# Performance work log

Measured on AMD Instinct MI355X. Metric: run time of the kernel, lower is better.

Reference implementation:

```python
import jax, jax.numpy as jnp
import numpy as np

BN_EPS = 1e-5

def _conv1d(x, w, b, pad):
    # x: [B, C_in, L], w: [C_out, C_in, K]
    y = jax.lax.conv_general_dilated(x, w, (1,), [(pad, pad)],
                                     dimension_numbers=('NCH', 'OIH', 'NCH'))
    return y + b[None, :, None]

def _gru_dir(x, wih, whh, bih, bhh, reverse):
    # x: [B, L, I]; wih: [3H, I]; whh: [3H, H] (PyTorch GRU gate order r,z,n)
    H = whh.shape[1]
    gx = jnp.einsum('bli,gi->blg', x, wih) + bih  # [B, L, 3H]
    gx = jnp.swapaxes(gx, 0, 1)                    # [L, B, 3H]
    if reverse:
        gx = gx[::-1]
    def step(h, xt):
        gh = h @ whh.T + bhh
        xr, xz, xn = jnp.split(xt, 3, axis=-1)
        hr, hz, hn = jnp.split(gh, 3, axis=-1)
        r = jax.nn.sigmoid(xr + hr)
        z = jax.nn.sigmoid(xz + hz)
        n = jnp.tanh(xn + r * hn)
        h = (1 - z) * n + z * h
        return h, h
    h0 = jnp.zeros((x.shape[0], H), x.dtype)
    _, hs = jax.lax.scan(step, h0, gx)
    if reverse:
        hs = hs[::-1]
    return jnp.swapaxes(hs, 0, 1)  # [B, L, H]

def _bigru(x, wih, whh, bih, bhh):
    f = _gru_dir(x, wih[0], whh[0], bih[0], bhh[0], False)
    b = _gru_dir(x, wih[1], whh[1], bih[1], bhh[1], True)
    return jnp.concatenate([f, b], axis=-1)

def _bn_eval(x, gamma, beta):
    # eval-mode BatchNorm1d with running_mean=0, running_var=1
    return x / jnp.sqrt(1.0 + BN_EPS) * gamma + beta

def _forward(wd_emb, pos_emb, conv_w2, conv_b2, conv_w3, conv_b3, conv_w4, conv_b4,
             wd_wih0, wd_whh0, wd_bih0, wd_bhh0, wd_wih1, wd_whh1, wd_bih1, wd_bhh1,
             pos_wih0, pos_whh0, pos_bih0, pos_bhh0, pos_wih1, pos_whh1, pos_bih1, pos_bhh1,
             squish_w, atten_proj, posfc_gamma, posfc_beta, posfc_w, posfc_b,
             fc1_w, fc1_b, fc_gamma, fc_beta, fc2_w, fc2_b, wd, pos):
    we = wd_emb[wd]    # [B, L, D]
    pe = pos_emb[pos]  # [B, L, D]
    x = jnp.swapaxes(we, 1, 2)  # [B, D, L]
    L = x.shape[-1]
    # parallel conv branches, truncated to min length L, concat -> 144 channels
    c2 = _conv1d(x, conv_w2, conv_b2, 1)[:, :, :L]
    c3 = _conv1d(x, conv_w3, conv_b3, 1)[:, :, :L]
    c4 = _conv1d(x, conv_w4, conv_b4, 2)[:, :, :L]
    feat = jnp.swapaxes(jnp.concatenate([c2, c3, c4], axis=1), 1, 2)  # [B, L, 144]
    # 2-layer bidirectional GRUs (hidden=3; dropout disabled at eval)
    wd_out = _bigru(_bigru(feat, wd_wih0, wd_whh0, wd_bih0, wd_bhh0),
                    wd_wih1, wd_whh1, wd_bih1, wd_bhh1)   # [B, L, 6]
    pos_out = _bigru(_bigru(pe, pos_wih0, pos_whh0, pos_bih0, pos_bhh0),
                     pos_wih1, pos_whh1, pos_bih1, pos_bhh1)  # [B, L, 6]
    # word attention (vectorized version of batch_matmul/attention_matmul loops)
    squish = jnp.tanh(wd_out @ squish_w)        # [B, L, 6]
    att = squish @ atten_proj                    # [B, L, 1]
    attn = jax.nn.softmax(att, axis=1)           # softmax over seq dim
    wd_atten = jnp.sum(wd_out * attn, axis=1)    # [B, 6]
    # auxiliary pos head
    ph = jax.nn.relu(_bn_eval(pos_out[:, -1, :], posfc_gamma, posfc_beta))
    auxi = jax.nn.softmax(ph @ posfc_w.T + posfc_b, axis=-1)  # [B, 3]
    # main head
    comb = jnp.concatenate([wd_atten, auxi], axis=1)  # [B, 9]
    h = jax.nn.relu(_bn_eval(comb @ fc1_w.T + fc1_b, fc_gamma, fc_beta))
    logits = jax.nn.softmax(h @ fc2_w.T + fc2_b, axis=-1)     # [B, 6]
    return logits, auxi

def setup_inputs() -> dict:
    key = jax.random.key(0)
    B, L, D, H, V, P = 512, 512, 100, 3, 23757, 57
    G = 3 * H  # 9
    keys = iter(jax.random.split(key, 48))
    def nrm(shape, s=0.1):
        return jax.random.normal(next(keys), shape, jnp.float32) * s
    inp = {}
    inp['wd'] = jax.random.randint(next(keys), (B, L), 0, V)
    inp['pos'] = jax.random.randint(next(keys), (B, L), 0, P)
    inp['wd_emb'] = nrm((V, D), 1.0)
    inp['pos_emb'] = nrm((P, D), 1.0)
    inp['conv_w2'] = nrm((48, D, 2)); inp['conv_b2'] = nrm((48,))
    inp['conv_w3'] = nrm((48, D, 3)); inp['conv_b3'] = nrm((48,))
    inp['conv_w4'] = nrm((48, D, 4)); inp['conv_b4'] = nrm((48,))
    inp['wd_wih0'] = nrm((2, G, 144)); inp['wd_whh0'] = nrm((2, G, H))
    inp['wd_bih0'] = nrm((2, G));      inp['wd_bhh0'] = nrm((2, G))
    inp['wd_wih1'] = nrm((2, G, 2 * H)); inp['wd_whh1'] = nrm((2, G, H))
    inp['wd_bih1'] = nrm((2, G));        inp['wd_bhh1'] = nrm((2, G))
    inp['pos_wih0'] = nrm((2, G, D));    inp['pos_whh0'] = nrm((2, G, H))
    inp['pos_bih0'] = nrm((2, G));       inp['pos_bhh0'] = nrm((2, G))
    inp['pos_wih1'] = nrm((2, G, 2 * H)); inp['pos_whh1'] = nrm((2, G, H))
    inp['pos_bih1'] = nrm((2, G));        inp['pos_bhh1'] = nrm((2, G))
    inp['squish_w'] = nrm((2 * H, 2 * H), 1.0)
    inp['atten_proj'] = nrm((2 * H, 1), 1.0)
    inp['posfc_gamma'] = jnp.ones((2 * H,), jnp.float32)
    inp['posfc_beta'] = jnp.zeros((2 * H,), jnp.float32)
    inp['posfc_w'] = nrm((3, 2 * H)); inp['posfc_b'] = nrm((3,))
    inp['fc1_w'] = nrm((128, 9)); inp['fc1_b'] = nrm((128,))
    inp['fc_gamma'] = jnp.ones((128,), jnp.float32)
    inp['fc_beta'] = jnp.zeros((128,), jnp.float32)
    inp['fc2_w'] = nrm((6, 128)); inp['fc2_b'] = nrm((6,))
    return inp

def reference(wd, pos, wd_emb, pos_emb, conv_w2, conv_b2, conv_w3, conv_b3, conv_w4, conv_b4,
              wd_wih0, wd_whh0, wd_bih0, wd_bhh0, wd_wih1, wd_whh1, wd_bih1, wd_bhh1,
              pos_wih0, pos_whh0, pos_bih0, pos_bhh0, pos_wih1, pos_whh1, pos_bih1, pos_bhh1,
              squish_w, atten_proj, posfc_gamma, posfc_beta, posfc_w, posfc_b,
              fc1_w, fc1_b, fc_gamma, fc_beta, fc2_w, fc2_b):
    return _forward(wd_emb, pos_emb, conv_w2, conv_b2, conv_w3, conv_b3, conv_w4, conv_b4,
                    wd_wih0, wd_whh0, wd_bih0, wd_bhh0, wd_wih1, wd_whh1, wd_bih1, wd_bhh1,
                    pos_wih0, pos_whh0, pos_bih0, pos_bhh0, pos_wih1, pos_whh1, pos_bih1, pos_bhh1,
                    squish_w, atten_proj, posfc_gamma, posfc_beta, posfc_w, posfc_b,
                    fc1_w, fc1_b, fc_gamma, fc_beta, fc2_w, fc2_b, wd, pos)
```

## Files before the change

kernel.cpp:

```cpp
#include <hip/hip_runtime.h>
#include <hip/hip_fp16.h>
#include <math.h>

#define BB 512
#define LL 512
#define VV 23757
#define PP 57

#define L2E  1.4426950408889634f
#define NL2E (-1.4426950408889634f)
#define TL2E 2.8853900817779268f

__device__ __forceinline__ float rcp_(float x) { return __builtin_amdgcn_rcpf(x); }
__device__ __forceinline__ float exp2_(float x) { return __builtin_amdgcn_exp2f(x); }
__device__ __forceinline__ float tanh_(float x) { return 1.f - 2.f * rcp_(exp2_(TL2E * x) + 1.f); }

__device__ __forceinline__ float gscale(int dg) {
    int g = (dg % 9) / 3;
    return g == 2 ? TL2E : NL2E;
}
__device__ __forceinline__ int is_rz(int dg) { return ((dg % 9) / 3) < 2; }

template <int K>
__device__ __forceinline__ float qb(float x) {
    constexpr int ctrl = K * 0x55;
    return __int_as_float(__builtin_amdgcn_update_dpp(0, __float_as_int(x), ctrl, 0xF, 0xF, true));
}

struct F3 { float r, z, n; };
struct H4 { __half2 a, b; };

__global__ void k_build_tables(const float* __restrict__ wd_wih0, const float* __restrict__ wd_bih0,
                               const float* __restrict__ wd_bhh0,
                               const float* __restrict__ cw2, const float* __restrict__ cb2,
                               const float* __restrict__ cw3, const float* __restrict__ cb3,
                               const float* __restrict__ cw4, const float* __restrict__ cb4,
                               const float* __restrict__ pos_emb,
                               const float* __restrict__ pos_wih0, const float* __restrict__ pos_bih0,
                               const float* __restrict__ pos_bhh0,
                               const float* __restrict__ wd_wih1, const float* __restrict__ wd_bih1,
                               const float* __restrict__ wd_bhh1,
                               const float* __restrict__ pos_wih1, const float* __restrict__ pos_bih1,
                               const float* __restrict__ pos_bhh1,
                               float* __restrict__ E, float* __restrict__ beff, float* __restrict__ Gp,
                               float* __restrict__ wih1t, float* __restrict__ bih1t)
{
    int idx = blockIdx.x * blockDim.x + threadIdx.x;
    if (idx < 7200) {
        int d  = idx % 100;
        int tt = (idx / 100) % 4;
        int dg = idx / 400;
        const float* wih = wd_wih0 + dg * 144;
        float acc = 0.f;
        if (tt == 0) {
            for (int o = 0; o < 48; ++o) acc += wih[96 + o] * cw4[o * 400 + d * 4 + 0];
        } else if (tt == 1) {
            for (int o = 0; o < 48; ++o) acc += wih[o]      * cw2[o * 200 + d * 2 + 0];
            for (int o = 0; o < 48; ++o) acc += wih[48 + o] * cw3[o * 300 + d * 3 + 0];
            for (int o = 0; o < 48; ++o) acc += wih[96 + o] * cw4[o * 400 + d * 4 + 1];
        } else if (tt == 2) {
            for (int o = 0; o < 48; ++o) acc += wih[o]      * cw2[o * 200 + d * 2 + 1];
            for (int o = 0; o < 48; ++o) acc += wih[48 + o] * cw3[o * 300 + d * 3 + 1];
            for (int o = 0; o < 48; ++o) acc += wih[96 + o] * cw4[o * 400 + d * 4 + 2];
        } else {
            for (int o = 0; o < 48; ++o) acc += wih[48 + o] * cw3[o * 300 + d * 3 + 2];
            for (int o = 0; o < 48; ++o) acc += wih[96 + o] * cw4[o * 400 + d * 4 + 3];
        }
        E[idx] = acc;
    } else if (idx < 7218) {
        int dg = idx - 7200;
        float acc = wd_bih0[dg];
        for (int o = 0; o < 48; ++o) acc += wd_wih0[dg * 144 + o]      * cb2[o];
        for (int o = 0; o < 48; ++o) acc += wd_wih0[dg * 144 + 48 + o] * cb3[o];
        for (int o = 0; o < 48; ++o) acc += wd_wih0[dg * 144 + 96 + o] * cb4[o];
        if (is_rz(dg)) acc += wd_bhh0[dg];
        beff[dg] = gscale(dg) * acc;
    } else if (idx < 8244) {
        int k = idx - 7218;
        int dg = k % 18;
        int p  = k / 18;
        float acc = pos_bih0[dg];
        for (int d = 0; d < 100; ++d) acc += pos_emb[p * 100 + d] * pos_wih0[dg * 100 + d];
        if (is_rz(dg)) acc += pos_bhh0[dg];
        Gp[p * 18 + dg] = gscale(dg) * acc;
    } else if (idx < 8352) {
        int i = idx - 8244; int dg = i / 6;
        wih1t[i] = gscale(dg) * wd_wih1[i];
    } else if (idx < 8370) {
        int dg = idx - 8352;
        float a = wd_bih1[dg] + (is_rz(dg) ? wd_bhh1[dg] : 0.f);
        bih1t[dg] = gscale(dg) * a;
    } else if (idx < 8478) {
        int i = idx - 8370; int dg = i / 6;
        wih1t[108 + i] = gscale(dg) * pos_wih1[i];
    } else if (idx < 8496) {
        int dg = idx - 8478;
        float a = pos_bih1[dg] + (is_rz(dg) ? pos_bhh1[dg] : 0.f);
        bih1t[18 + dg] = gscale(dg) * a;
    }
}

__global__ void __launch_bounds__(256) k_build_P(const float* __restrict__ wd_emb,
                                                 const float* __restrict__ E,
                                                 __half* __restrict__ P16)
{
    __shared__ float sEt[7200];
    for (int i = threadIdx.x; i < 7200; i += 256) {
        int d = i % 100, r = i / 100;
        int tt = r / 18, dg = r % 18;
        sEt[d * 72 + r] = E[dg * 400 + tt * 100 + d];
    }
    __syncthreads();
    int T = blockIdx.x * 256 + threadIdx.x;
    int og = T & 7;
    int vb = T >> 3;
    int v0 = vb * 4;
    if (v0 >= VV) return;
    int vlim = VV - 1 - v0;
    float gs[9];
#pragma unroll
    for (int k = 0; k < 9; ++k) {
        int dg = (og * 9 + k) % 18;
        gs[k] = ((dg % 9) / 3 == 2) ? TL2E : NL2E;
    }
    float acc[4][9];
#pragma unroll
    for (int vi = 0; vi < 4; ++vi)
#pragma unroll
        for (int k = 0; k < 9; ++k) acc[vi][k] = 0.f;

    const float* e0 = wd_emb + (size_t)v0 * 100;
#pragma unroll 1
    for (int d4 = 0; d4 < 25; ++d4) {
        float4 ev[4];
#pragma unroll
        for (int vi = 0; vi < 4; ++vi) {
            int vv = vi <= vlim ? vi : vlim;
            ev[vi] = *(const float4*)(e0 + vv * 100 + d4 * 4);
        }
#pragma unroll
        for (int dd = 0; dd < 4; ++dd) {
            int d = d4 * 4 + dd;
            const float* et = sEt + d * 72 + og * 9;
            float em0 = ((const float*)&ev[0])[dd];
            float em1 = ((const float*)&ev[1])[dd];
            float em2 = ((const float*)&ev[2])[dd];
            float em3 = ((const float*)&ev[3])[dd];
#pragma unroll
            for (int k = 0; k < 9; ++k) {
                float e = et[k];
                acc[0][k] = fmaf(em0, e, acc[0][k]);
                acc[1][k] = fmaf(em1, e, acc[1][k]);
                acc[2][k] = fmaf(em2, e, acc[2][k]);
                acc[3][k] = fmaf(em3, e, acc[3][k]);
            }
        }
    }
#pragma unroll
    for (int vi = 0; vi < 4; ++vi) {
        if (vi <= vlim) {
            __half* p = P16 + (size_t)(v0 + vi) * 72 + og * 9;
#pragma unroll
            for (int k = 0; k < 9; ++k) p[k] = __float2half_rn(gs[k] * acc[vi][k]);
        }
    }
}

__global__ void k_gather(const int* __restrict__ wd, const int* __restrict__ pos,
                         const __half* __restrict__ P16, const float* __restrict__ beff,
                         const float* __restrict__ Gp, char* __restrict__ gxh)
{
    int idx = blockIdx.x * blockDim.x + threadIdx.x;
    if (idx >= 2 * BB * LL) return;
    int branch = idx >= BB * LL;
    int k = idx - branch * BB * LL;
    int l = k % LL, b = k / LL;

    float v[18];
    if (!branch) {
#pragma unroll
        for (int i = 0; i < 18; ++i) v[i] = beff[i];
        const int* row = wd + b * LL;
#pragma unroll
        for (int t = 0; t < 4; ++t) {
            int ll = l - 2 + t;
            if (ll >= 0 && ll < LL) {
                const __half2* p = (const __half2*)(P16 + (size_t)row[ll] * 72 + t * 18);
#pragma unroll
                for (int i = 0; i < 9; ++i) {
                    float2 f = __half22float2(p[i]);
                    v[2 * i] += f.x;
                    v[2 * i + 1] += f.y;
                }
            }
        }
    } else {
        const float* p = Gp + pos[k] * 18;
#pragma unroll
        for (int i = 0; i < 18; ++i) v[i] = p[i];
    }
    char* g0 = gxh + ((size_t)((branch * 2 + 0) * BB + b) * LL + l) * 24;
    char* g1 = gxh + ((size_t)((branch * 2 + 1) * BB + b) * LL + l) * 24;
#pragma unroll
    for (int j = 0; j < 3; ++j) {
        H4 w0, w1;
        w0.a = __floats2half2_rn(v[j], v[3 + j]);
        w0.b = __floats2half2_rn(v[6 + j], 0.f);
        w1.a = __floats2half2_rn(v[9 + j], v[12 + j]);
        w1.b = __floats2half2_rn(v[15 + j], 0.f);
        *(H4*)(g0 + j * 8) = w0;
        *(H4*)(g1 + j * 8) = w1;
    }
}

#define GRU_CORE(GR, GZ, GN)                                                  \
    {                                                                         \
        float h0_ = qb<0>(h), h1_ = qb<1>(h), h2_ = qb<2>(h);                 \
        float sr_ = fmaf(wr0, h0_, fmaf(wr1, h1_, fmaf(wr2, h2_, (GR))));     \
        float sz_ = fmaf(wz0, h0_, fmaf(wz1, h1_, fmaf(wz2, h2_, (GZ))));     \
        float g3_ = fmaf(wn0, h0_, fmaf(wn1, h1_, fmaf(wn2, h2_, bnx)));      \
        float r_ = rcp_(1.f + exp2_(sr_));                                    \
        float z_ = rcp_(1.f + exp2_(sz_));                                    \
        float u_ = rcp_(1.f + exp2_(fmaf(r_, g3_, (GN))));                    \
        float n_ = fmaf(-2.f, u_, 1.f);                                       \
        h = fmaf(z_, h - n_, n_);                                             \
    }

__global__ void __launch_bounds__(64) k_scan0(
        const char* __restrict__ gxh, char* __restrict__ out0h,
        const float* __restrict__ whhA, const float* __restrict__ bhhA,
        const float* __restrict__ whhB, const float* __restrict__ bhhB)
{
    __shared__ float lbuf[8 * 81];
    int lane = threadIdx.x;
    int c = lane >> 2, sub = lane & 3;
    int jj = sub < 3 ? sub : 2;
    int chain = blockIdx.x;
    int branch = chain >> 10;
    int rem = chain & 1023;
    int dir = rem >> 9;

    const float* whh = (branch ? whhB : whhA) + dir * 27;
    const float* bhh = (branch ? bhhB : bhhA) + dir * 9;

    float wr0 = NL2E * whh[jj * 3 + 0], wr1 = NL2E * whh[jj * 3 + 1], wr2 = NL2E * whh[jj * 3 + 2];
    float wz0 = NL2E * whh[(3 + jj) * 3 + 0], wz1 = NL2E * whh[(3 + jj) * 3 + 1], wz2 = NL2E * whh[(3 + jj) * 3 + 2];
    float wn0 = TL2E * whh[(6 + jj) * 3 + 0], wn1 = TL2E * whh[(6 + jj) * 3 + 1], wn2 = TL2E * whh[(6 + jj) * 3 + 2];
    float bnx = TL2E * bhh[6 + jj];

    const int OMAX = 511 * 24;
    int t0 = c * 32 - 24;
    int sstp = dir ? -24 : 24;
    int off = dir ? (OMAX - t0 * 24) : t0 * 24;
    const char* gxc = gxh + (size_t)chain * (LL * 24) + jj * 8;

#define LDP(P) { int a_ = min(max(off, 0), OMAX); P = *(const H4*)(gxc + a_); off += sstp; }
    H4 p0, p1, p2, p3, p4, p5, p6, p7;
    LDP(p0) LDP(p1) LDP(p2) LDP(p3) LDP(p4) LDP(p5) LDP(p6) LDP(p7)

    char* ob = out0h + (size_t)chain * (LL * 8) + sub * 16;
    int wa = c * 5 + sub;

    float h = 0.f;
#define WSTEP(P) { H4 hv_ = P; LDP(P); float2 fa_ = __half22float2(hv_.a); \
                   float fn_ = __half22float2(hv_.b).x; GRU_CORE(fa_.x, fa_.y, fn_) }
#define RSTEP(P, S) { WSTEP(P) lbuf[(S) * 81 + wa] = h; }
#define FLUSH0(TB)                                                            \
    {                                                                         \
        int tbase = (TB);                                                     \
        int l0 = dir ? (LL - 1 - tbase - 7) : tbase;                          \
        _Pragma("unroll")                                                     \
        for (int i = 0; i < 2; ++i) {                                         \
            int lofs = sub * 2 + i;                                           \
            int s = dir ? (7 - lofs) : lofs;                                  \
            H4 hv;                                                            \
            hv.a = __floats2half2_rn(lbuf[s * 81 + c * 5 + 0],                \
                                     lbuf[s * 81 + c * 5 + 1]);               \
            hv.b = __floats2half2_rn(lbuf[s * 81 + c * 5 + 2],                \
                                     lbuf[s * 81 + c * 5 + 3]);               \
            *(H4*)(ob + (size_t)l0 * 8 + i * 8) = hv;                         \
        }                                                                     \
    }

    for (int g = 0; g < 3; ++g) {
        WSTEP(p0) WSTEP(p1) WSTEP(p2) WSTEP(p3) WSTEP(p4) WSTEP(p5) WSTEP(p6) WSTEP(p7)
    }
    h = c ? h : 0.f;

    for (int g = 0; g < 4; ++g) {
        RSTEP(p0, 0) RSTEP(p1, 1) RSTEP(p2, 2) RSTEP(p3, 3)
        RSTEP(p4, 4) RSTEP(p5, 5) RSTEP(p6, 6) RSTEP(p7, 7)
        FLUSH0(t0 + 24 + g * 8)
    }
#undef LDP
#undef WSTEP
#undef RSTEP
#undef FLUSH0
}

__global__ void __launch_bounds__(64) k_scan1(
        const char* __restrict__ out0h, char* __restrict__ out1h,
        const float* __restrict__ whhA, const float* __restrict__ bhhA,
        const float* __restrict__ whhB, const float* __restrict__ bhhB,
        const float* __restrict__ wih1t, const float* __restrict__ bih1t)
{
    __shared__ float lbuf[8 * 81];
    int lane = threadIdx.x;
    int c = lane >> 2, sub = lane & 3;
    int jj = sub < 3 ? sub : 2;
    int chain = blockIdx.x;
    int branch = chain >> 10;
    int rem = chain & 1023;
    int dir = rem >> 9;
    int b = rem & 511;

    const float* whh = (branch ? whhB : whhA) + dir * 27;
    const float* bhh = (branch ? bhhB : bhhA) + dir * 9;

    float wr0 = NL2E * whh[jj * 3 + 0], wr1 = NL2E * whh[jj * 3 + 1], wr2 = NL2E * whh[jj * 3 + 2];
    float wz0 = NL2E * whh[(3 + jj) * 3 + 0], wz1 = NL2E * whh[(3 + jj) * 3 + 1], wz2 = NL2E * whh[(3 + jj) * 3 + 2];
    float wn0 = TL2E * whh[(6 + jj) * 3 + 0], wn1 = TL2E * whh[(6 + jj) * 3 + 1], wn2 = TL2E * whh[(6 + jj) * 3 + 2];
    float bnx = TL2E * bhh[6 + jj];

    const float* Wb = wih1t + branch * 108;
    const float* Bv = bih1t + branch * 18;
    int dgr = dir * 9 + jj, dgz = dgr + 3, dgn = dgr + 6;
    float Wr0 = Wb[dgr * 6 + 0], Wr1 = Wb[dgr * 6 + 1], Wr2 = Wb[dgr * 6 + 2];
    float Wr3 = Wb[dgr * 6 + 3], Wr4 = Wb[dgr * 6 + 4], Wr5 = Wb[dgr * 6 + 5];
    float Wz0 = Wb[dgz * 6 + 0], Wz1 = Wb[dgz * 6 + 1], Wz2 = Wb[dgz * 6 + 2];
    float Wz3 = Wb[dgz * 6 + 3], Wz4 = Wb[dgz * 6 + 4], Wz5 = Wb[dgz * 6 + 5];
    float Wn0 = Wb[dgn * 6 + 0], Wn1 = Wb[dgn * 6 + 1], Wn2 = Wb[dgn * 6 + 2];
    float Wn3 = Wb[dgn * 6 + 3], Wn4 = Wb[dgn * 6 + 4], Wn5 = Wb[dgn * 6 + 5];
    float Br = Bv[dgr], Bz = Bv[dgz], Bn = Bv[dgn];

    const char* o0c = out0h + (size_t)((branch * 2 + 0) * BB + b) * (LL * 8);
    const char* o1c = out0h + (size_t)((branch * 2 + 1) * BB + b) * (LL * 8);

    const int OMAX = 511 * 8;
    int t0 = c * 32 - 24;
    int sstp = dir ? -8 : 8;
    int off = dir ? (OMAX - t0 * 8) : t0 * 8;

#define LDF(F, Q) { int a_ = min(max(off, 0), OMAX); F = *(const H4*)(o0c + a_); \
                    Q = *(const H4*)(o1c + a_); off += sstp; }
    H4 f0, f1, f2, f3, f4, f5, f6, f7;
    H4 q0, q1, q2, q3, q4, q5, q6, q7;
    LDF(f0, q0) LDF(f1, q1) LDF(f2, q2) LDF(f3, q3)
    LDF(f4, q4) LDF(f5, q5) LDF(f6, q6) LDF(f7, q7)

    char* ob = out1h + (size_t)chain * (LL * 8) + sub * 16;
    int wa = c * 5 + sub;

    float h = 0.f;
#define PRJ_STEP(FV, QV)                                                      \
    {                                                                         \
        float2 fa_ = __half22float2((FV).a);                                  \
        float fn_ = __half22float2((FV).b).x;                                 \
        float2 qa_ = __half22float2((QV).a);                                  \
        float qn_ = __half22float2((QV).b).x;                                 \
        float gr_ = fmaf(fa_.x, Wr0, fmaf(fa_.y, Wr1, fmaf(fn_, Wr2, Br)));   \
        gr_ = fmaf(qa_.x, Wr3, fmaf(qa_.y, Wr4, fmaf(qn_, Wr5, gr_)));        \
        float gz_ = fmaf(fa_.x, Wz0, fmaf(fa_.y, Wz1, fmaf(fn_, Wz2, Bz)));   \
        gz_ = fmaf(qa_.x, Wz3, fmaf(qa_.y, Wz4, fmaf(qn_, Wz5, gz_)));        \
        float gn_ = fmaf(fa_.x, Wn0, fmaf(fa_.y, Wn1, fmaf(fn_, Wn2, Bn)));   \
        gn_ = fmaf(qa_.x, Wn3, fmaf(qa_.y, Wn4, fmaf(qn_, Wn5, gn_)));        \
        GRU_CORE(gr_, gz_, gn_)                                               \
    }
#define WSTEP(F, Q) { H4 fv_ = F, qv_ = Q; LDF(F, Q); PRJ_STEP(fv_, qv_) }
#define RSTEP(F, Q, S) { WSTEP(F, Q) lbuf[(S) * 81 + wa] = h; }
#define FLUSH1(TB)                                                            \
    {                                                                         \
        int tbase = (TB);                                                     \
        int l0 = dir ? (LL - 1 - tbase - 7) : tbase;                          \
        _Pragma("unroll")                                                     \
        for (int i = 0; i < 2; ++i) {                                         \
            int lofs = sub * 2 + i;                                           \
            int s = dir ? (7 - lofs) : lofs;                                  \
            H4 hv;                                                            \
            hv.a = __floats2half2_rn(lbuf[s * 81 + c * 5 + 0],                \
                                     lbuf[s * 81 + c * 5 + 1]);               \
            hv.b = __floats2half2_rn(lbuf[s * 81 + c * 5 + 2],                \
                                     lbuf[s * 81 + c * 5 + 3]);               \
            *(H4*)(ob + (size_t)l0 * 8 + i * 8) = hv;                         \
        }                                                                     \
    }

    for (int g = 0; g < 3; ++g) {
        WSTEP(f0, q0) WSTEP(f1, q1) WSTEP(f2, q2) WSTEP(f3, q3)
        WSTEP(f4, q4) WSTEP(f5, q5) WSTEP(f6, q6) WSTEP(f7, q7)
    }
    h = c ? h : 0.f;

    for (int g = 0; g < 4; ++g) {
        RSTEP(f0, q0, 0) RSTEP(f1, q1, 1) RSTEP(f2, q2, 2) RSTEP(f3, q3, 3)
        RSTEP(f4, q4, 4) RSTEP(f5, q5, 5) RSTEP(f6, q6, 6) RSTEP(f7, q7, 7)
        FLUSH1(t0 + 24 + g * 8)
    }
#undef LDF
#undef PRJ_STEP
#undef WSTEP
#undef RSTEP
#undef FLUSH1
}

__global__ void k_head(const char* __restrict__ out1h,
                       const float* __restrict__ sw, const float* __restrict__ ap,
                       const float* __restrict__ pg, const float* __restrict__ pb,
                       const float* __restrict__ pw, const float* __restrict__ pbias,
                       const float* __restrict__ f1w, const float* __restrict__ f1b,
                       const float* __restrict__ fg, const float* __restrict__ fb,
                       const float* __restrict__ f2w, const float* __restrict__ f2b,
                       float* __restrict__ out)
{
    int b = blockIdx.x;
    int lane = threadIdx.x;
    __shared__ float ssw[36], sap[6], sph[6], scomb[9], sh[128], sl[6], se[6];
    const float BN = 0.9999950000374997f;

    if (lane < 36) ssw[lane] = sw[lane];
    if (lane < 6) {
        sap[lane] = ap[lane];
        H4 pf = *(const H4*)(out1h + ((size_t)((2 * BB) + b) * LL + 511) * 8);
        H4 pq = *(const H4*)(out1h + ((size_t)((3 * BB) + b) * LL + 511) * 8);
        float2 fa = __half22float2(pf.a); float fn = __half22float2(pf.b).x;
        float2 ba = __half22float2(pq.a); float bn = __half22float2(pq.b).x;
        float v = lane == 0 ? fa.x : lane == 1 ? fa.y : lane == 2 ? fn
                : lane == 3 ? ba.x : lane == 4 ? ba.y : bn;
        float x = v * BN * pg[lane] + pb[lane];
        sph[lane] = fmaxf(x, 0.f);
    }
    __syncthreads();

    const char* F = out1h + (size_t)b * (LL * 8);
    const char* Bw = out1h + (size_t)(BB + b) * (LL * 8);

    float att[8];
    float mx = -1e30f;
#pragma unroll
    for (int k = 0; k < 8; ++k) {
        int l = lane + 64 * k;
        H4 f4 = *(const H4*)(F + l * 8);
        H4 b4 = *(const H4*)(Bw + l * 8);
        float2 fa = __half22float2(f4.a); float fn = __half22float2(f4.b).x;
        float2 ba = __half22float2(b4.a); float bn = __half22float2(b4.b).x;
        float r0 = fa.x, r1 = fa.y, r2 = fn, r3 = ba.x, r4 = ba.y, r5 = bn;
        float a = 0.f;
#pragma unroll
        for (int j = 0; j < 6; ++j) {
            float s = r0 * ssw[0 * 6 + j] + r1 * ssw[1 * 6 + j] + r2 * ssw[2 * 6 + j] +
                      r3 * ssw[3 * 6 + j] + r4 * ssw[4 * 6 + j] + r5 * ssw[5 * 6 + j];
            a += sap[j] * tanh_(s);
        }
        att[k] = a;
        mx = fmaxf(mx, a);
    }
#pragma unroll
    for (int off = 32; off; off >>= 1) mx = fmaxf(mx, __shfl_xor(mx, off));
    float e[8];
    float sum = 0.f;
#pragma unroll
    for (int k = 0; k < 8; ++k) { e[k] = exp2_(L2E * (att[k] - mx)); sum += e[k]; }
#pragma unroll
    for (int off = 32; off; off >>= 1) sum += __shfl_xor(sum, off);

    float acc[6] = {0.f, 0.f, 0.f, 0.f, 0.f, 0.f};
#pragma unroll
    for (int k = 0; k < 8; ++k) {
        int l = lane + 64 * k;
        H4 f4 = *(const H4*)(F + l * 8);
        H4 b4 = *(const H4*)(Bw + l * 8);
        float2 fa = __half22float2(f4.a); float fn = __half22float2(f4.b).x;
        float2 ba = __half22float2(b4.a); float bn = __half22float2(b4.b).x;
        acc[0] += e[k] * fa.x; acc[1] += e[k] * fa.y; acc[2] += e[k] * fn;
        acc[3] += e[k] * ba.x; acc[4] += e[k] * ba.y; acc[5] += e[k] * bn;
    }
#pragma unroll
    for (int j = 0; j < 6; ++j) {
#pragma unroll
        for (int off = 32; off; off >>= 1) acc[j] += __shfl_xor(acc[j], off);
    }
    if (lane < 6) scomb[lane] = acc[lane] / sum;
    __syncthreads();

    if (lane == 0) {
        float a[3];
#pragma unroll
        for (int j = 0; j < 3; ++j) {
            float t = pbias[j];
#pragma unroll
            for (int i = 0; i < 6; ++i) t += sph[i] * pw[j * 6 + i];
            a[j] = t;
        }
        float m = fmaxf(a[0], fmaxf(a[1], a[2]));
        float e0 = exp2_(L2E * (a[0] - m)), e1 = exp2_(L2E * (a[1] - m)), e2 = exp2_(L2E * (a[2] - m));
        float s = e0 + e1 + e2;
        float x0 = e0 / s, x1 = e1 / s, x2 = e2 / s;
        scomb[6] = x0; scomb[7] = x1; scomb[8] = x2;
        out[BB * 6 + b * 3 + 0] = x0;
        out[BB * 6 + b * 3 + 1] = x1;
        out[BB * 6 + b * 3 + 2] = x2;
    }
    __syncthreads();
    for (int o = lane; o < 128; o += 64) {
        float t = f1b[o];
#pragma unroll
        for (int k = 0; k < 9; ++k) t += scomb[k] * f1w[o * 9 + k];
        float x = t * BN * fg[o] + fb[o];
        sh[o] = fmaxf(x, 0.f);
    }
    __syncthreads();
    if (lane < 6) {
        float t = f2b[lane];
        for (int k = 0; k < 128; ++k) t += sh[k] * f2w[lane * 128 + k];
        sl[lane] = t;
    }
    __syncthreads();
    if (lane < 6) {
        float m = sl[0];
#pragma unroll
        for (int j = 1; j < 6; ++j) m = fmaxf(m, sl[j]);
        se[lane] = exp2_(L2E * (sl[lane] - m));
    }
    __syncthreads();
    if (lane < 6) {
        float s = se[0] + se[1] + se[2] + se[3] + se[4] + se[5];
        out[b * 6 + lane] = se[lane] / s;
    }
}

extern "C" void kernel_launch(void* const* d_in, const int* in_sizes, int n_in,
                              void* d_out, int out_size, void* d_ws, size_t ws_size,
                              hipStream_t stream)
{
    const int* wd  = (const int*)d_in[0];
    const int* pos = (const int*)d_in[1];
    const float* wd_emb  = (const float*)d_in[2];
    const float* pos_emb = (const float*)d_in[3];
    const float* cw2 = (const float*)d_in[4];  const float* cb2 = (const float*)d_in[5];
    const float* cw3 = (const float*)d_in[6];  const float* cb3 = (const float*)d_in[7];
    const float* cw4 = (const float*)d_in[8];  const float* cb4 = (const float*)d_in[9];
    const float* wd_wih0 = (const float*)d_in[10]; const float* wd_whh0 = (const float*)d_in[11];
    const float* wd_bih0 = (const float*)d_in[12]; const float* wd_bhh0 = (const float*)d_in[13];
    const float* wd_wih1 = (const float*)d_in[14]; const float* wd_whh1 = (const float*)d_in[15];
    const float* wd_bih1 = (const float*)d_in[16]; const float* wd_bhh1 = (const float*)d_in[17];
    const float* pos_wih0 = (const float*)d_in[18]; const float* pos_whh0 = (const float*)d_in[19];
    const float* pos_bih0 = (const float*)d_in[20]; const float* pos_bhh0 = (const float*)d_in[21];
    const float* pos_wih1 = (const float*)d_in[22]; const float* pos_whh1 = (const float*)d_in[23];
    const float* pos_bih1 = (const float*)d_in[24]; const float* pos_bhh1 = (const float*)d_in[25];
    const float* squish_w   = (const float*)d_in[26];
    const float* atten_proj = (const float*)d_in[27];
    const float* posfc_gamma = (const float*)d_in[28]; const float* posfc_beta = (const float*)d_in[29];
    const float* posfc_w = (const float*)d_in[30]; const float* posfc_b = (const float*)d_in[31];
    const float* fc1_w = (const float*)d_in[32]; const float* fc1_b = (const float*)d_in[33];
    const float* fc_gamma = (const float*)d_in[34]; const float* fc_beta = (const float*)d_in[35];
    const float* fc2_w = (const float*)d_in[36]; const float* fc2_b = (const float*)d_in[37];

    float* ws = (float*)d_ws;
    size_t off = 0;
    __half* P16 = (__half*)(ws + off); off += (size_t)VV * 36 + 8;
    char* gxh = (char*)(ws + off);   off += (size_t)4 * BB * LL * 6;
    char* out0h = (char*)(ws + off); off += (size_t)4 * BB * LL * 2;
    char* out1h = (char*)(ws + off); off += (size_t)4 * BB * LL * 2;
    float* Etab = ws + off;   off += 7200;
    float* beff = ws + off;   off += 32;
    float* Gp = ws + off;     off += PP * 18 + 14;
    float* wih1t = ws + off;  off += 216;
    float* bih1t = ws + off;  off += 40;

    k_build_tables<<<(8496 + 255) / 256, 256, 0, stream>>>(
        wd_wih0, wd_bih0, wd_bhh0, cw2, cb2, cw3, cb3, cw4, cb4,
        pos_emb, pos_wih0, pos_bih0, pos_bhh0,
        wd_wih1, wd_bih1, wd_bhh1, pos_wih1, pos_bih1, pos_bhh1,
        Etab, beff, Gp, wih1t, bih1t);
    {
        int vb = (VV + 3) / 4;
        int threads = vb * 8;
        k_build_P<<<(threads + 255) / 256, 256, 0, stream>>>(wd_emb, Etab, P16);
    }
    k_gather<<<(2 * BB * LL + 255) / 256, 256, 0, stream>>>(wd, pos, P16, beff, Gp, gxh);
    k_scan0<<<2048, 64, 0, stream>>>(gxh, out0h, wd_whh0, wd_bhh0, pos_whh0, pos_bhh0);
    k_scan1<<<2048, 64, 0, stream>>>(out0h, out1h, wd_whh1, wd_bhh1, pos_whh1, pos_bhh1,
                                     wih1t, bih1t);
    k_head<<<BB, 64, 0, stream>>>(out1h, squish_w, atten_proj, posfc_gamma, posfc_beta,
                                  posfc_w, posfc_b, fc1_w, fc1_b, fc_gamma, fc_beta,
                                  fc2_w, fc2_b, (float*)d_out);
}
```

Before: 87.98 us.

## Fuse table-building into P-projection kernel and shorten scan warmup

Merges the table-building kernel into the P-table kernel. Each block now recomputes the conv-folded E matrix straight into shared memory, and extra blocks compute the bias and pos tables, which removes one launch and the E round-trip through global memory. The layer-1 input weights are scaled inline inside the scan kernel instead of in a precomputed table. The chunked-scan warmup is cut from 24 to 16 steps in both GRU layers, which trims serial work but may lower accuracy at chunk boundaries. Every P block now repeats the 7200-entry E computation, adding redundant arithmetic per block.

```diff
diff --git a/kernel.cpp b/kernel.cpp
--- a/kernel.cpp
+++ b/kernel.cpp
@@ -6,6 +6,7 @@
 #define LL 512
 #define VV 23757
 #define PP 57
+#define NBP 186
 
 #define L2E  1.4426950408889634f
 #define NL2E (-1.4426950408889634f)
@@ -27,88 +28,72 @@
     return __int_as_float(__builtin_amdgcn_update_dpp(0, __float_as_int(x), ctrl, 0xF, 0xF, true));
 }
 
-struct F3 { float r, z, n; };
 struct H4 { __half2 a, b; };
 
-__global__ void k_build_tables(const float* __restrict__ wd_wih0, const float* __restrict__ wd_bih0,
-                               const float* __restrict__ wd_bhh0,
-                               const float* __restrict__ cw2, const float* __restrict__ cb2,
-                               const float* __restrict__ cw3, const float* __restrict__ cb3,
-                               const float* __restrict__ cw4, const float* __restrict__ cb4,
-                               const float* __restrict__ pos_emb,
-                               const float* __restrict__ pos_wih0, const float* __restrict__ pos_bih0,
-                               const float* __restrict__ pos_bhh0,
-                               const float* __restrict__ wd_wih1, const float* __restrict__ wd_bih1,
-                               const float* __restrict__ wd_bhh1,
-                               const float* __restrict__ pos_wih1, const float* __restrict__ pos_bih1,
-                               const float* __restrict__ pos_bhh1,
-                               float* __restrict__ E, float* __restrict__ beff, float* __restrict__ Gp,
-                               float* __restrict__ wih1t, float* __restrict__ bih1t)
-{
-    int idx = blockIdx.x * blockDim.x + threadIdx.x;
-    if (idx < 7200) {
-        int d  = idx % 100;
-        int tt = (idx / 100) % 4;
-        int dg = idx / 400;
-        const float* wih = wd_wih0 + dg * 144;
-        float acc = 0.f;
-        if (tt == 0) {
-            for (int o = 0; o < 48; ++o) acc += wih[96 + o] * cw4[o * 400 + d * 4 + 0];
-        } else if (tt == 1) {
-            for (int o = 0; o < 48; ++o) acc += wih[o]      * cw2[o * 200 + d * 2 + 0];
-            for (int o = 0; o < 48; ++o) acc += wih[48 + o] * cw3[o * 300 + d * 3 + 0];
-            for (int o = 0; o < 48; ++o) acc += wih[96 + o] * cw4[o * 400 + d * 4 + 1];
-        } else if (tt == 2) {
-            for (int o = 0; o < 48; ++o) acc += wih[o]      * cw2[o * 200 + d * 2 + 1];
-            for (int o = 0; o < 48; ++o) acc += wih[48 + o] * cw3[o * 300 + d * 3 + 1];
-            for (int o = 0; o < 48; ++o) acc += wih[96 + o] * cw4[o * 400 + d * 4 + 2];
-        } else {
-            for (int o = 0; o < 48; ++o) acc += wih[48 + o] * cw3[o * 300 + d * 3 + 2];
-            for (int o = 0; o < 48; ++o) acc += wih[96 + o] * cw4[o * 400 + d * 4 + 3];
-        }
-        E[idx] = acc;
-    } else if (idx < 7218) {
-        int dg = idx - 7200;
-        float acc = wd_bih0[dg];
-        for (int o = 0; o < 48; ++o) acc += wd_wih0[dg * 144 + o]      * cb2[o];
-        for (int o = 0; o < 48; ++o) acc += wd_wih0[dg * 144 + 48 + o] * cb3[o];
-        for (int o = 0; o < 48; ++o) acc += wd_wih0[dg * 144 + 96 + o] * cb4[o];
-        if (is_rz(dg)) acc += wd_bhh0[dg];
-        beff[dg] = gscale(dg) * acc;
-    } else if (idx < 8244) {
-        int k = idx - 7218;
-        int dg = k % 18;
-        int p  = k / 18;
-        float acc = pos_bih0[dg];
-        for (int d = 0; d < 100; ++d) acc += pos_emb[p * 100 + d] * pos_wih0[dg * 100 + d];
-        if (is_rz(dg)) acc += pos_bhh0[dg];
-        Gp[p * 18 + dg] = gscale(dg) * acc;
-    } else if (idx < 8352) {
-        int i = idx - 8244; int dg = i / 6;
-        wih1t[i] = gscale(dg) * wd_wih1[i];
-    } else if (idx < 8370) {
-        int dg = idx - 8352;
-        float a = wd_bih1[dg] + (is_rz(dg) ? wd_bhh1[dg] : 0.f);
-        bih1t[dg] = gscale(dg) * a;
-    } else if (idx < 8478) {
-        int i = idx - 8370; int dg = i / 6;
-        wih1t[108 + i] = gscale(dg) * pos_wih1[i];
-    } else if (idx < 8496) {
-        int dg = idx - 8478;
-        float a = pos_bih1[dg] + (is_rz(dg) ? pos_bhh1[dg] : 0.f);
-        bih1t[18 + dg] = gscale(dg) * a;
-    }
-}
-
-__global__ void __launch_bounds__(256) k_build_P(const float* __restrict__ wd_emb,
-                                                 const float* __restrict__ E,
-                                                 __half* __restrict__ P16)
-{
+__device__ __forceinline__ float e_entry(const float* __restrict__ wd_wih0,
+                                         const float* __restrict__ cw2,
+                                         const float* __restrict__ cw3,
+                                         const float* __restrict__ cw4,
+                                         int dg, int tt, int d)
+{
+    const float* wih = wd_wih0 + dg * 144;
+    float acc = 0.f;
+    if (tt == 0) {
+        for (int o = 0; o < 48; ++o) acc += wih[96 + o] * cw4[o * 400 + d * 4 + 0];
+    } else if (tt == 1) {
+        for (int o = 0; o < 48; ++o) acc += wih[o]      * cw2[o * 200 + d * 2 + 0];
+        for (int o = 0; o < 48; ++o) acc += wih[48 + o] * cw3[o * 300 + d * 3 + 0];
+        for (int o = 0; o < 48; ++o) acc += wih[96 + o] * cw4[o * 400 + d * 4 + 1];
+    } else if (tt == 2) {
+        for (int o = 0; o < 48; ++o) acc += wih[o]      * cw2[o * 200 + d * 2 + 1];
+        for (int o = 0; o < 48; ++o) acc += wih[48 + o] * cw3[o * 300 + d * 3 + 1];
+        for (int o = 0; o < 48; ++o) acc += wih[96 + o] * cw4[o * 400 + d * 4 + 2];
+    } else {
+        for (int o = 0; o < 48; ++o) acc += wih[48 + o] * cw3[o * 300 + d * 3 + 2];
+        for (int o = 0; o < 48; ++o) acc += wih[96 + o] * cw4[o * 400 + d * 4 + 3];
+    }
+    return acc;
+}
+
+__global__ void __launch_bounds__(256) k_prep(
+        const float* __restrict__ wd_emb,
+        const float* __restrict__ wd_wih0, const float* __restrict__ wd_bih0,
+        const float* __restrict__ wd_bhh0,
+        const float* __restrict__ cw2, const float* __restrict__ cb2,
+        const float* __restrict__ cw3, const float* __restrict__ cb3,
+        const float* __restrict__ cw4, const float* __restrict__ cb4,
+        const float* __restrict__ pos_emb,
+        const float* __restrict__ pos_wih0, const float* __restrict__ pos_bih0,
+        const float* __restrict__ pos_bhh0,
+        __half* __restrict__ P16, float* __restrict__ beff, float* __restrict__ Gp)
+{
+    if (blockIdx.x >= NBP) {
+        int idx = (blockIdx.x - NBP) * 256 + threadIdx.x;
+        if (idx < 18) {
+            int dg = idx;
+            float acc = wd_bih0[dg];
+            for (int o = 0; o < 48; ++o) acc += wd_wih0[dg * 144 + o]      * cb2[o];
+            for (int o = 0; o < 48; ++o) acc += wd_wih0[dg * 144 + 48 + o] * cb3[o];
+            for (int o = 0; o < 48; ++o) acc += wd_wih0[dg * 144 + 96 + o] * cb4[o];
+            if (is_rz(dg)) acc += wd_bhh0[dg];
+            beff[dg] = gscale(dg) * acc;
+        } else if (idx < 18 + PP * 18) {
+            int k = idx - 18;
+            int dg = k % 18;
+            int p  = k / 18;
+            float acc = pos_bih0[dg];
+            for (int d = 0; d < 100; ++d) acc += pos_emb[p * 100 + d] * pos_wih0[dg * 100 + d];
+            if (is_rz(dg)) acc += pos_bhh0[dg];
+            Gp[p * 18 + dg] = gscale(dg) * acc;
+        }
+        return;
+    }
+
     __shared__ float sEt[7200];
     for (int i = threadIdx.x; i < 7200; i += 256) {
         int d = i % 100, r = i / 100;
         int tt = r / 18, dg = r % 18;
-        sEt[d * 72 + r] = E[dg * 400 + tt * 100 + d];
+        sEt[d * 72 + r] = e_entry(wd_wih0, cw2, cw3, cw4, dg, tt, d);
     }
     __syncthreads();
     int T = blockIdx.x * 256 + threadIdx.x;
@@ -249,7 +234,7 @@
     float bnx = TL2E * bhh[6 + jj];
 
     const int OMAX = 511 * 24;
-    int t0 = c * 32 - 24;
+    int t0 = c * 32 - 16;
     int sstp = dir ? -24 : 24;
     int off = dir ? (OMAX - t0 * 24) : t0 * 24;
     const char* gxc = gxh + (size_t)chain * (LL * 24) + jj * 8;
@@ -282,7 +267,7 @@
         }                                                                     \
     }
 
-    for (int g = 0; g < 3; ++g) {
+    for (int g = 0; g < 2; ++g) {
         WSTEP(p0) WSTEP(p1) WSTEP(p2) WSTEP(p3) WSTEP(p4) WSTEP(p5) WSTEP(p6) WSTEP(p7)
     }
     h = c ? h : 0.f;
@@ -290,7 +275,7 @@
     for (int g = 0; g < 4; ++g) {
         RSTEP(p0, 0) RSTEP(p1, 1) RSTEP(p2, 2) RSTEP(p3, 3)
         RSTEP(p4, 4) RSTEP(p5, 5) RSTEP(p6, 6) RSTEP(p7, 7)
-        FLUSH0(t0 + 24 + g * 8)
+        FLUSH0(t0 + 16 + g * 8)
     }
 #undef LDP
 #undef WSTEP
@@ -302,7 +287,8 @@
         const char* __restrict__ out0h, char* __restrict__ out1h,
         const float* __restrict__ whhA, const float* __restrict__ bhhA,
         const float* __restrict__ whhB, const float* __restrict__ bhhB,
-        const float* __restrict__ wih1t, const float* __restrict__ bih1t)
+        const float* __restrict__ wihA, const float* __restrict__ bihA,
+        const float* __restrict__ wihB, const float* __restrict__ bihB)
 {
     __shared__ float lbuf[8 * 81];
     int lane = threadIdx.x;
@@ -322,22 +308,25 @@
     float wn0 = TL2E * whh[(6 + jj) * 3 + 0], wn1 = TL2E * whh[(6 + jj) * 3 + 1], wn2 = TL2E * whh[(6 + jj) * 3 + 2];
     float bnx = TL2E * bhh[6 + jj];
 
-    const float* Wb = wih1t + branch * 108;
-    const float* Bv = bih1t + branch * 18;
+    const float* wih = branch ? wihB : wihA;
+    const float* bih = branch ? bihB : bihA;
+    const float* bh1 = branch ? bhhB : bhhA;
     int dgr = dir * 9 + jj, dgz = dgr + 3, dgn = dgr + 6;
-    float Wr0 = Wb[dgr * 6 + 0], Wr1 = Wb[dgr * 6 + 1], Wr2 = Wb[dgr * 6 + 2];
-    float Wr3 = Wb[dgr * 6 + 3], Wr4 = Wb[dgr * 6 + 4], Wr5 = Wb[dgr * 6 + 5];
-    float Wz0 = Wb[dgz * 6 + 0], Wz1 = Wb[dgz * 6 + 1], Wz2 = Wb[dgz * 6 + 2];
-    float Wz3 = Wb[dgz * 6 + 3], Wz4 = Wb[dgz * 6 + 4], Wz5 = Wb[dgz * 6 + 5];
-    float Wn0 = Wb[dgn * 6 + 0], Wn1 = Wb[dgn * 6 + 1], Wn2 = Wb[dgn * 6 + 2];
-    float Wn3 = Wb[dgn * 6 + 3], Wn4 = Wb[dgn * 6 + 4], Wn5 = Wb[dgn * 6 + 5];
-    float Br = Bv[dgr], Bz = Bv[dgz], Bn = Bv[dgn];
+    float Wr0 = NL2E * wih[dgr * 6 + 0], Wr1 = NL2E * wih[dgr * 6 + 1], Wr2 = NL2E * wih[dgr * 6 + 2];
+    float Wr3 = NL2E * wih[dgr * 6 + 3], Wr4 = NL2E * wih[dgr * 6 + 4], Wr5 = NL2E * wih[dgr * 6 + 5];
+    float Wz0 = NL2E * wih[dgz * 6 + 0], Wz1 = NL2E * wih[dgz * 6 + 1], Wz2 = NL2E * wih[dgz * 6 + 2];
+    float Wz3 = NL2E * wih[dgz * 6 + 3], Wz4 = NL2E * wih[dgz * 6 + 4], Wz5 = NL2E * wih[dgz * 6 + 5];
+    float Wn0 = TL2E * wih[dgn * 6 + 0], Wn1 = TL2E * wih[dgn * 6 + 1], Wn2 = TL2E * wih[dgn * 6 + 2];
+    float Wn3 = TL2E * wih[dgn * 6 + 3], Wn4 = TL2E * wih[dgn * 6 + 4], Wn5 = TL2E * wih[dgn * 6 + 5];
+    float Br = NL2E * (bih[dgr] + bh1[dgr]);
+    float Bz = NL2E * (bih[dgz] + bh1[dgz]);
+    float Bn = TL2E * bih[dgn];
 
     const char* o0c = out0h + (size_t)((branch * 2 + 0) * BB + b) * (LL * 8);
     const char* o1c = out0h + (size_t)((branch * 2 + 1) * BB + b) * (LL * 8);
 
     const int OMAX = 511 * 8;
-    int t0 = c * 32 - 24;
+    int t0 = c * 32 - 16;
     int sstp = dir ? -8 : 8;
     int off = dir ? (OMAX - t0 * 8) : t0 * 8;
 
@@ -385,7 +374,7 @@
         }                                                                     \
     }
 
-    for (int g = 0; g < 3; ++g) {
+    for (int g = 0; g < 2; ++g) {
         WSTEP(f0, q0) WSTEP(f1, q1) WSTEP(f2, q2) WSTEP(f3, q3)
         WSTEP(f4, q4) WSTEP(f5, q5) WSTEP(f6, q6) WSTEP(f7, q7)
     }
@@ -394,7 +383,7 @@
     for (int g = 0; g < 4; ++g) {
         RSTEP(f0, q0, 0) RSTEP(f1, q1, 1) RSTEP(f2, q2, 2) RSTEP(f3, q3, 3)
         RSTEP(f4, q4, 4) RSTEP(f5, q5, 5) RSTEP(f6, q6, 6) RSTEP(f7, q7, 7)
-        FLUSH1(t0 + 24 + g * 8)
+        FLUSH1(t0 + 16 + g * 8)
     }
 #undef LDF
 #undef PRJ_STEP
@@ -558,29 +547,19 @@
     float* ws = (float*)d_ws;
     size_t off = 0;
     __half* P16 = (__half*)(ws + off); off += (size_t)VV * 36 + 8;
-    char* gxh = (char*)(ws + off);   off += (size_t)4 * BB * LL * 6;
     char* out0h = (char*)(ws + off); off += (size_t)4 * BB * LL * 2;
     char* out1h = (char*)(ws + off); off += (size_t)4 * BB * LL * 2;
-    float* Etab = ws + off;   off += 7200;
+    char* gxh = (char*)(ws + off);   off += (size_t)4 * BB * LL * 6;
     float* beff = ws + off;   off += 32;
     float* Gp = ws + off;     off += PP * 18 + 14;
-    float* wih1t = ws + off;  off += 216;
-    float* bih1t = ws + off;  off += 40;
-
-    k_build_tables<<<(8496 + 255) / 256, 256, 0, stream>>>(
-        wd_wih0, wd_bih0, wd_bhh0, cw2, cb2, cw3, cb3, cw4, cb4,
-        pos_emb, pos_wih0, pos_bih0, pos_bhh0,
-        wd_wih1, wd_bih1, wd_bhh1, pos_wih1, pos_bih1, pos_bhh1,
-        Etab, beff, Gp, wih1t, bih1t);
-    {
-        int vb = (VV + 3) / 4;
-        int threads = vb * 8;
-        k_build_P<<<(threads + 255) / 256, 256, 0, stream>>>(wd_emb, Etab, P16);
-    }
+
+    k_prep<<<NBP + 5, 256, 0, stream>>>(
+        wd_emb, wd_wih0, wd_bih0, wd_bhh0, cw2, cb2, cw3, cb3, cw4, cb4,
+        pos_emb, pos_wih0, pos_bih0, pos_bhh0, P16, beff, Gp);
     k_gather<<<(2 * BB * LL + 255) / 256, 256, 0, stream>>>(wd, pos, P16, beff, Gp, gxh);
     k_scan0<<<2048, 64, 0, stream>>>(gxh, out0h, wd_whh0, wd_bhh0, pos_whh0, pos_bhh0);
     k_scan1<<<2048, 64, 0, stream>>>(out0h, out1h, wd_whh1, wd_bhh1, pos_whh1, pos_bhh1,
-                                     wih1t, bih1t);
+                                     wd_wih1, wd_bih1, pos_wih1, pos_bih1);
     k_head<<<BB, 64, 0, stream>>>(out1h, squish_w, atten_proj, posfc_gamma, posfc_beta,
                                   posfc_w, posfc_b, fc1_w, fc1_b, fc_gamma, fc_beta,
                                   fc2_w, fc2_b, (float*)d_out);
```

New measurement: 223.7 us. 2.54x slower.
